# Kernel optimization log

Hardware: AMD Instinct MI355X
Metric: run time of the kernel (lower is better)

## Reference

```python
import jax, jax.numpy as jnp
import numpy as np

B, N, H, HS = 8, 96, 8, 32
NS = H * HS  # 256, also ES
EPS = 1e-5


def _linear(x, w, b):
    return x @ w + b  # w: [in, out]


def _ln(x, g, b):
    m = jnp.mean(x, axis=-1, keepdims=True)
    v = jnp.var(x, axis=-1, keepdims=True)
    return (x - m) * jax.lax.rsqrt(v + EPS) * g + b


def _sep_n(x):  # [B,N,NS] -> [B,H,N,HS]
    b, n, _ = x.shape
    return x.reshape(b, n, H, HS).transpose(0, 2, 1, 3)


def _sep_e(x):  # [B,N,N,ES] -> [B,H,N,N,HS]
    b, n, _, _ = x.shape
    return x.reshape(b, n, n, H, HS).transpose(0, 3, 1, 2, 4)


def setup_inputs() -> dict:
    key = jax.random.key(0)
    ks = jax.random.split(key, 32)
    s = 1.0 / np.sqrt(NS)
    d = {
        "node_tensors": jax.random.normal(ks[0], (B, N, NS), jnp.float32),
        "edge_tensors": jax.random.normal(ks[1], (B, N, N, NS), jnp.float32),
    }
    names = ["Wn", "We", "Wn1", "Wn2", "Wee"]
    for i, nm in enumerate(names):
        d[nm + "_w"] = jax.random.uniform(ks[2 + 2 * i], (3, NS, NS), jnp.float32, -s, s)
        d[nm + "_b"] = jax.random.uniform(ks[3 + 2 * i], (3, NS), jnp.float32, -s, s)
    for i, nm in enumerate(["NL1", "NL2", "EL1", "EL2"]):
        d[nm + "_w"] = jax.random.uniform(ks[12 + 2 * i], (NS, NS), jnp.float32, -s, s)
        d[nm + "_b"] = jax.random.uniform(ks[13 + 2 * i], (NS,), jnp.float32, -s, s)
    d["NLN1_g"] = jnp.ones((NS,), jnp.float32)
    d["NLN1_b"] = jnp.zeros((NS,), jnp.float32)
    d["ELN1_g"] = jnp.ones((NS,), jnp.float32)
    d["ELN1_b"] = jnp.zeros((NS,), jnp.float32)
    return d


def _forward(node_tensors, edge_tensors, Wn_w, Wn_b, We_w, We_b, Wn1_w, Wn1_b,
             Wn2_w, Wn2_b, Wee_w, Wee_b, NL1_w, NL1_b, NL2_w, NL2_b,
             EL1_w, EL1_b, EL2_w, EL2_b, NLN1_g, NLN1_b, ELN1_g, ELN1_b):
    scale = 1.0 / jnp.sqrt(jnp.float32(HS))
    b = node_tensors.shape[0]

    # --- node attention ---
    eQ = _sep_e(_linear(edge_tensors, We_w[0], We_b[0]))
    eK = _sep_e(_linear(edge_tensors, We_w[1], We_b[1]))
    eV = _sep_e(_linear(edge_tensors, We_w[2], We_b[2]))
    nQ = _sep_n(_linear(node_tensors, Wn_w[0], Wn_b[0]))
    nK = _sep_n(_linear(node_tensors, Wn_w[1], Wn_b[1]))
    nV = _sep_n(_linear(node_tensors, Wn_w[2], Wn_b[2]))

    Q = eQ + nQ[:, :, :, None, :]          # [B,H,N,N,HS]
    K = eK + nK[:, :, None, :, :]
    scores = jnp.einsum('bhijc,bhijc->bhij', Q, K) * scale
    attn = jax.nn.softmax(scores, axis=-1)
    V = eV + nV[:, :, None, :, :]
    new_nodes = jnp.einsum('bhij,bhijc->bhic', attn, V)   # [B,H,N,HS]
    attw = new_nodes.transpose(0, 2, 1, 3).reshape(b, N, NS)

    res = _linear(jax.nn.relu(_linear(attw, NL1_w, NL1_b)), NL2_w, NL2_b)
    node_out = _ln(node_tensors + res, NLN1_g, NLN1_b)

    # --- edge update ---
    n1Q = _sep_n(_linear(node_out, Wn1_w[0], Wn1_b[0]))
    n1K = _sep_n(_linear(node_out, Wn1_w[1], Wn1_b[1]))
    n1V = _sep_n(_linear(node_out, Wn1_w[2], Wn1_b[2]))
    n2Q = _sep_n(_linear(node_out, Wn2_w[0], Wn2_b[0]))
    n2K = _sep_n(_linear(node_out, Wn2_w[1], Wn2_b[1]))
    n2V = _sep_n(_linear(node_out, Wn2_w[2], Wn2_b[2]))
    eQe = _sep_e(_linear(edge_tensors, Wee_w[0], Wee_b[0]))
    eKe = _sep_e(_linear(edge_tensors, Wee_w[1], Wee_b[1]))
    eVe = _sep_e(_linear(edge_tensors, Wee_w[2], Wee_b[2]))

    Qe = eQe + n1Q[:, :, :, None, :] + n2Q[:, :, None, :, :]
    Ke = eKe + n1K[:, :, :, None, :] + n2K[:, :, None, :, :]
    se = jnp.einsum('bhijc,bhijc->bhij', Qe, Ke) * scale
    attn_e = jax.nn.silu(se)                               # [B,H,N,N]
    Ve = eVe + n1V[:, :, :, None, :] + n2V[:, :, None, :, :]
    new_edges = attn_e[..., None] * Ve                     # [B,H,N,N,HS]
    attw_e = new_edges.transpose(0, 2, 3, 1, 4).reshape(b, N, N, NS)

    res_e = _linear(jax.nn.relu(_linear(attw_e, EL1_w, EL1_b)), EL2_w, EL2_b)
    edge_out = _ln(edge_tensors + res_e, ELN1_g, ELN1_b)
    return node_out, edge_out


def reference(node_tensors, edge_tensors, Wn_w, Wn_b, We_w, We_b, Wn1_w, Wn1_b,
              Wn2_w, Wn2_b, Wee_w, Wee_b, NL1_w, NL1_b, NL2_w, NL2_b,
              EL1_w, EL1_b, EL2_w, EL2_b, NLN1_g, NLN1_b, ELN1_g, ELN1_b):
    return _forward(node_tensors, edge_tensors, Wn_w, Wn_b, We_w, We_b,
                    Wn1_w, Wn1_b, Wn2_w, Wn2_b, Wee_w, Wee_b, NL1_w, NL1_b,
                    NL2_w, NL2_b, EL1_w, EL1_b, EL2_w, EL2_b,
                    NLN1_g, NLN1_b, ELN1_g, ELN1_b)
```

## Files before the change

### kernel.cpp

```cpp
#include <hip/hip_runtime.h>


#define DI __device__ __forceinline__

typedef float f32x4 __attribute__((ext_vector_type(4)));
typedef short bf16x8 __attribute__((ext_vector_type(8)));

DI unsigned short f2bf(float f) {
  union { float f; unsigned u; } v; v.f = f;
  return (unsigned short)((v.u + 0x7FFFu + ((v.u >> 16) & 1u)) >> 16);
}
DI float bf2f(unsigned short h) {
  union { unsigned u; float f; } v; v.u = ((unsigned)h) << 16;
  return v.f;
}

#define LDE 264
#define SCALE 0.17677669529663687f

#define MFMA(A, B, C) __builtin_amdgcn_mfma_f32_16x16x32_bf16((A), (B), (C), 0, 0, 0)

__global__ __launch_bounds__(256)
void prep_frags(const float* __restrict__ We_w, const float* __restrict__ Wee_w,
                const float* __restrict__ EL1_w, const float* __restrict__ EL2_w,
                const float* __restrict__ NL1_w, const float* __restrict__ NL2_w,
                const float* __restrict__ Wn1_w, const float* __restrict__ Wn2_w,
                const float* __restrict__ Wn_w,
                unsigned short* __restrict__ fb)
{
  __shared__ float Wl[32 * 256];
  const int t = threadIdx.x;
  const int blk = blockIdx.x, kt = blk & 7, ms = blk >> 3;
  const float* src; unsigned short* dst; int NT, ntbase;
  if (ms < 3)       { src = We_w  + ms * 65536;        dst = fb;           NT = 48; ntbase = ms * 16; }
  else if (ms < 6)  { src = Wee_w + (ms - 3) * 65536;  dst = fb + 196608;  NT = 48; ntbase = (ms - 3) * 16; }
  else if (ms == 6) { src = EL1_w;                     dst = fb + 393216;  NT = 16; ntbase = 0; }
  else if (ms == 7) { src = EL2_w;                     dst = fb + 458752;  NT = 16; ntbase = 0; }
  else if (ms == 8) { src = NL1_w;                     dst = fb + 524288;  NT = 16; ntbase = 0; }
  else if (ms == 9) { src = NL2_w;                     dst = fb + 589824;  NT = 16; ntbase = 0; }
  else if (ms < 13) { src = Wn1_w + (ms - 10) * 65536; dst = fb + 655360;  NT = 48; ntbase = (ms - 10) * 16; }
  else if (ms < 16) { src = Wn2_w + (ms - 13) * 65536; dst = fb + 851968;  NT = 48; ntbase = (ms - 13) * 16; }
  else              { src = Wn_w  + (ms - 16) * 65536; dst = fb + 1048576; NT = 48; ntbase = (ms - 16) * 16; }
  for (int u = t; u < 32 * 64; u += 256) {
    const int r = u >> 6, c4 = (u & 63) << 2;
    *(float4*)(Wl + r * 256 + c4) = *(const float4*)(src + (kt * 32 + r) * 256 + c4);
  }
  __syncthreads();
  for (int u = t; u < 16 * 64; u += 256) {
    const int ntl = u >> 6, l = u & 63;
    const int kb = (l >> 4) << 3, c = ntl * 16 + (l & 15);
    unsigned short tmp[8];
    #pragma unroll
    for (int i = 0; i < 8; ++i) tmp[i] = f2bf(Wl[(kb + i) * 256 + c]);
    const int nt = ntbase + ntl;
    *(uint4*)(dst + ((size_t)(kt * NT + nt) * 64 + l) * 8) = *(const uint4*)tmp;
  }
}

__global__ __launch_bounds__(256)
void node_qkv(const float* __restrict__ node, const unsigned short* __restrict__ WnF,
              const float* __restrict__ Wb, float* __restrict__ nQ,
              float* __restrict__ nK, float* __restrict__ nV)
{
  __shared__ unsigned short Xl[16 * LDE];
  const int t = threadIdx.x, lane = t & 63, w = t >> 6;
  const int rb = blockIdx.x, r0 = rb * 16;
  const int b = rb / 6, nbase = (rb % 6) * 16;

  for (int u = t; u < 16 * 64; u += 256) {
    const int j = u >> 6, gg = u & 63;
    const float4 v = *(const float4*)(node + (size_t)(r0 + j) * 256 + gg * 4);
    const unsigned lo = (unsigned)f2bf(v.x) | ((unsigned)f2bf(v.y) << 16);
    const unsigned hi = (unsigned)f2bf(v.z) | ((unsigned)f2bf(v.w) << 16);
    *(uint2*)(Xl + j * LDE + gg * 4) = make_uint2(lo, hi);
  }
  __syncthreads();

  const f32x4 z = {0.f, 0.f, 0.f, 0.f};
  bf16x8 xfr[8];
  #pragma unroll
  for (int kt = 0; kt < 8; ++kt)
    xfr[kt] = *(const bf16x8*)(Xl + (lane & 15) * LDE + ((lane >> 4) << 3) + kt * 32);
  f32x4 ac[12] = {z, z, z, z, z, z, z, z, z, z, z, z};
  __builtin_amdgcn_s_setprio(1);
  for (int kt = 0; kt < 8; ++kt) {
    #pragma unroll
    for (int m = 0; m < 12; ++m) {
      const int nt = w * 12 + m;
      const bf16x8 bf = *(const bf16x8*)(WnF + ((kt * 48 + nt) * 64 + lane) * 8);
      ac[m] = MFMA(xfr[kt], bf, ac[m]);
    }
  }
  __builtin_amdgcn_s_setprio(0);
  #pragma unroll
  for (int m = 0; m < 12; ++m) {
    const int colg = (w * 12 + m) * 16 + (lane & 15);
    const int q = colg >> 8, cn = colg & 255, h = cn >> 5, c = cn & 31;
    float* o = (q == 0) ? nQ : (q == 1) ? nK : nV;
    const float bv = Wb[colg];
    #pragma unroll
    for (int r = 0; r < 4; ++r) {
      const int j = ((lane >> 4) << 2) + r;
      o[((b * 8 + h) * 96 + nbase + j) * 32 + c] = ac[m][r] + bv;
    }
  }
}

__global__ __launch_bounds__(512, 2)
void node_attn(const float* __restrict__ edge, const float* __restrict__ We_b,
               const unsigned short* __restrict__ WeF,
               const float* __restrict__ nQ, const float* __restrict__ nK,
               const float* __restrict__ nV, float* __restrict__ attw)
{
  __shared__ unsigned short Elds[96 * LDE];
  __shared__ float sc[768];
  __shared__ float nQp[256];
  __shared__ float bias[768];

  const int tid = threadIdx.x, lane = tid & 63, wid = tid >> 6;
  const int b = blockIdx.x & 7, i = blockIdx.x >> 3;
  const size_t bi = (size_t)(b * 96 + i);

  if (tid < 256) nQp[tid] = nQ[((b * 8 + (tid >> 5)) * 96 + i) * 32 + (tid & 31)];
  for (int u = tid; u < 768; u += 512) bias[u] = We_b[u];

  const float* Erow = edge + bi * 24576;
  for (int u = tid; u < 96 * 64; u += 512) {
    const int j = u >> 6, g = u & 63;
    const float4 v = *(const float4*)(Erow + j * 256 + g * 4);
    const unsigned lo = (unsigned)f2bf(v.x) | ((unsigned)f2bf(v.y) << 16);
    const unsigned hi = (unsigned)f2bf(v.z) | ((unsigned)f2bf(v.w) << 16);
    *(uint2*)(Elds + j * LDE + g * 4) = make_uint2(lo, hi);
  }
  __syncthreads();

  {
    const int h = wid;
    const unsigned short* wq0 = WeF + ((2 * h) * 64 + lane) * 8;
    const unsigned short* wq1 = WeF + ((2 * h + 1) * 64 + lane) * 8;
    const unsigned short* wk0 = WeF + ((16 + 2 * h) * 64 + lane) * 8;
    const unsigned short* wk1 = WeF + ((17 + 2 * h) * 64 + lane) * 8;
    const int c0 = h * 32 + (lane & 15), c1 = c0 + 16;
    const float qb0 = bias[c0] + nQp[c0], qb1 = bias[c1] + nQp[c1];
    const float kb0 = bias[256 + c0], kb1 = bias[256 + c1];
    for (int pass = 0; pass < 2; ++pass) {
      const f32x4 z = {0.f, 0.f, 0.f, 0.f};
      f32x4 aq0[3] = {z, z, z}, aq1[3] = {z, z, z}, ak0[3] = {z, z, z}, ak1[3] = {z, z, z};
      __builtin_amdgcn_s_setprio(1);
      for (int kt = 0; kt < 8; ++kt) {
        const bf16x8 b0 = *(const bf16x8*)(wq0 + kt * 24576);
        const bf16x8 b1 = *(const bf16x8*)(wq1 + kt * 24576);
        const bf16x8 b2 = *(const bf16x8*)(wk0 + kt * 24576);
        const bf16x8 b3 = *(const bf16x8*)(wk1 + kt * 24576);
        #pragma unroll
        for (int m = 0; m < 3; ++m) {
          const int mt = pass * 3 + m;
          const bf16x8 afr = *(const bf16x8*)(Elds + (mt * 16 + (lane & 15)) * LDE
                                              + ((lane >> 4) << 3) + kt * 32);
          aq0[m] = MFMA(afr, b0, aq0[m]);
          aq1[m] = MFMA(afr, b1, aq1[m]);
          ak0[m] = MFMA(afr, b2, ak0[m]);
          ak1[m] = MFMA(afr, b3, ak1[m]);
        }
      }
      __builtin_amdgcn_s_setprio(0);
      #pragma unroll
      for (int m = 0; m < 3; ++m) {
        const int mt = pass * 3 + m;
        float prod[4];
        #pragma unroll
        for (int r = 0; r < 4; ++r) {
          const int j = mt * 16 + ((lane >> 4) << 2) + r;
          const int g = ((b * 8 + h) * 96 + j) * 32;
          const float k0v = ak0[m][r] + kb0 + nK[g + (lane & 15)];
          const float k1v = ak1[m][r] + kb1 + nK[g + 16 + (lane & 15)];
          prod[r] = (aq0[m][r] + qb0) * k0v + (aq1[m][r] + qb1) * k1v;
        }
        #pragma unroll
        for (int mm = 1; mm < 16; mm <<= 1) {
          #pragma unroll
          for (int r = 0; r < 4; ++r) prod[r] += __shfl_xor(prod[r], mm, 64);
        }
        if ((lane & 15) == 0) {
          #pragma unroll
          for (int r = 0; r < 4; ++r)
            sc[h * 96 + mt * 16 + ((lane >> 4) << 2) + r] = prod[r];
        }
      }
    }
  }

  const f32x4 z = {0.f, 0.f, 0.f, 0.f};
  f32x4 accB[6][2] = {{z, z}, {z, z}, {z, z}, {z, z}, {z, z}, {z, z}};
  const int col0 = wid * 16 + (lane & 15), col1 = col0 + 128;
  const int h0 = col0 >> 5, cc0 = col0 & 31;
  const int h1 = col1 >> 5, cc1 = col1 & 31;
  {
    const unsigned short* wb0 = WeF + ((32 + wid) * 64 + lane) * 8;
    const unsigned short* wb1 = WeF + ((40 + wid) * 64 + lane) * 8;
    __builtin_amdgcn_s_setprio(1);
    for (int kt = 0; kt < 8; ++kt) {
      const bf16x8 b0 = *(const bf16x8*)(wb0 + kt * 24576);
      const bf16x8 b1 = *(const bf16x8*)(wb1 + kt * 24576);
      #pragma unroll
      for (int mt = 0; mt < 6; ++mt) {
        const bf16x8 afr = *(const bf16x8*)(Elds + (mt * 16 + (lane & 15)) * LDE
                                            + ((lane >> 4) << 3) + kt * 32);
        accB[mt][0] = MFMA(afr, b0, accB[mt][0]);
        accB[mt][1] = MFMA(afr, b1, accB[mt][1]);
      }
    }
    __builtin_amdgcn_s_setprio(0);
    const float base0 = bias[512 + col0], base1 = bias[512 + col1];
    #pragma unroll
    for (int mt = 0; mt < 6; ++mt) {
      #pragma unroll
      for (int r = 0; r < 4; ++r) {
        const int j = mt * 16 + ((lane >> 4) << 2) + r;
        accB[mt][0][r] += base0 + nV[((b * 8 + h0) * 96 + j) * 32 + cc0];
        accB[mt][1][r] += base1 + nV[((b * 8 + h1) * 96 + j) * 32 + cc1];
      }
    }
  }

  {
    const int h = wid;
    const float s0 = sc[h * 96 + lane] * SCALE;
    const float s1 = (lane < 32) ? sc[h * 96 + 64 + lane] * SCALE : -1e30f;
    float mx = fmaxf(s0, s1);
    #pragma unroll
    for (int m = 1; m < 64; m <<= 1) mx = fmaxf(mx, __shfl_xor(mx, m, 64));
    const float e0 = __expf(s0 - mx);
    const float e1 = (lane < 32) ? __expf(s1 - mx) : 0.f;
    float sm = e0 + e1;
    #pragma unroll
    for (int m = 1; m < 64; m <<= 1) sm += __shfl_xor(sm, m, 64);
    const float inv = 1.f / sm;
    sc[h * 96 + lane] = e0 * inv;
    if (lane < 32) sc[h * 96 + 64 + lane] = e1 * inv;
  }
  __syncthreads();

  {
    float nn[2] = {0.f, 0.f};
    #pragma unroll
    for (int mt = 0; mt < 6; ++mt) {
      #pragma unroll
      for (int r = 0; r < 4; ++r) {
        const int j = mt * 16 + ((lane >> 4) << 2) + r;
        nn[0] += sc[h0 * 96 + j] * accB[mt][0][r];
        nn[1] += sc[h1 * 96 + j] * accB[mt][1][r];
      }
    }
    #pragma unroll
    for (int s = 0; s < 2; ++s) {
      nn[s] += __shfl_xor(nn[s], 16, 64);
      nn[s] += __shfl_xor(nn[s], 32, 64);
    }
    if (lane < 16) {
      attw[bi * 256 + wid * 16 + lane] = nn[0];
      attw[bi * 256 + (wid + 8) * 16 + lane] = nn[1];
    }
  }
}

__global__ __launch_bounds__(256)
void node_tail(const float* __restrict__ attw, const float* __restrict__ node,
               const unsigned short* __restrict__ NL1F, const float* __restrict__ B1,
               const unsigned short* __restrict__ NL2F, const float* __restrict__ B2,
               const float* __restrict__ g, const float* __restrict__ be,
               const unsigned short* __restrict__ Wn1F, const float* __restrict__ P1b,
               const unsigned short* __restrict__ Wn2F, const float* __restrict__ P2b,
               float* __restrict__ node_out,
               float* __restrict__ n1Q, float* __restrict__ n1K, float* __restrict__ n1V,
               float* __restrict__ n2Q, float* __restrict__ n2K, float* __restrict__ n2V)
{
  __shared__ unsigned short Xl[16 * LDE];
  __shared__ unsigned short Hl[16 * LDE];
  __shared__ float bb[1024];
  __shared__ float psum[4][16], psq[4][16];
  __shared__ float statm[16], statr[16];

  const int t = threadIdx.x, lane = t & 63, w = t >> 6;
  const int ps = blockIdx.x & 1, rb = blockIdx.x >> 1;
  const int r0 = rb * 16, b = rb / 6, nbase = (rb % 6) * 16;

  bb[t] = B1[t]; bb[256 + t] = B2[t]; bb[512 + t] = g[t]; bb[768 + t] = be[t];

  for (int u = t; u < 16 * 64; u += 256) {
    const int j = u >> 6, gg = u & 63;
    const float4 v = *(const float4*)(attw + (size_t)(r0 + j) * 256 + gg * 4);
    const unsigned lo = (unsigned)f2bf(v.x) | ((unsigned)f2bf(v.y) << 16);
    const unsigned hi = (unsigned)f2bf(v.z) | ((unsigned)f2bf(v.w) << 16);
    *(uint2*)(Xl + j * LDE + gg * 4) = make_uint2(lo, hi);
  }
  __syncthreads();

  const f32x4 z = {0.f, 0.f, 0.f, 0.f};

  {
    f32x4 a1[4] = {z, z, z, z};
    for (int kt = 0; kt < 8; ++kt) {
      const bf16x8 afr = *(const bf16x8*)(Xl + (lane & 15) * LDE + ((lane >> 4) << 3) + kt * 32);
      #pragma unroll
      for (int p = 0; p < 4; ++p) {
        const bf16x8 bf = *(const bf16x8*)(NL1F + (((kt << 4) + (w * 4 + p)) * 64 + lane) * 8);
        a1[p] = MFMA(afr, bf, a1[p]);
      }
    }
    #pragma unroll
    for (int p = 0; p < 4; ++p) {
      const int col = (w * 4 + p) * 16 + (lane & 15);
      const float bv = bb[col];
      #pragma unroll
      for (int r = 0; r < 4; ++r) {
        const int j = ((lane >> 4) << 2) + r;
        Hl[j * LDE + col] = f2bf(fmaxf(a1[p][r] + bv, 0.f));
      }
    }
  }
  __syncthreads();

  float xv[4][4];
  {
    f32x4 a2[4] = {z, z, z, z};
    for (int kt = 0; kt < 8; ++kt) {
      const bf16x8 afr = *(const bf16x8*)(Hl + (lane & 15) * LDE + ((lane >> 4) << 3) + kt * 32);
      #pragma unroll
      for (int p = 0; p < 4; ++p) {
        const bf16x8 bf = *(const bf16x8*)(NL2F + (((kt << 4) + (w * 4 + p)) * 64 + lane) * 8);
        a2[p] = MFMA(afr, bf, a2[p]);
      }
    }
    #pragma unroll
    for (int p = 0; p < 4; ++p) {
      const int col = (w * 4 + p) * 16 + (lane & 15);
      const float bv = bb[256 + col];
      #pragma unroll
      for (int r = 0; r < 4; ++r) {
        const int j = ((lane >> 4) << 2) + r;
        xv[p][r] = a2[p][r] + bv + node[(size_t)(r0 + j) * 256 + col];
      }
    }
    #pragma unroll
    for (int r = 0; r < 4; ++r) {
      float s = 0.f, q = 0.f;
      #pragma unroll
      for (int p = 0; p < 4; ++p) { s += xv[p][r]; q += xv[p][r] * xv[p][r]; }
      #pragma unroll
      for (int m = 1; m < 16; m <<= 1) { s += __shfl_xor(s, m, 64); q += __shfl_xor(q, m, 64); }
      if ((lane & 15) == 0) {
        const int rl = ((lane >> 4) << 2) + r;
        psum[w][rl] = s; psq[w][rl] = q;
      }
    }
  }
  __syncthreads();
  if (t < 16) {
    const float s = psum[0][t] + psum[1][t] + psum[2][t] + psum[3][t];
    const float q = psq[0][t] + psq[1][t] + psq[2][t] + psq[3][t];
    const float mean = s * (1.f / 256.f);
    statm[t] = mean;
    statr[t] = rsqrtf(q * (1.f / 256.f) - mean * mean + 1e-5f);
  }
  __syncthreads();
  #pragma unroll
  for (int p = 0; p < 4; ++p) {
    const int col = (w * 4 + p) * 16 + (lane & 15);
    const float gv = bb[512 + col], bv = bb[768 + col];
    #pragma unroll
    for (int r = 0; r < 4; ++r) {
      const int j = ((lane >> 4) << 2) + r;
      const float o = (xv[p][r] - statm[j]) * statr[j] * gv + bv;
      if (ps == 0) node_out[(size_t)(r0 + j) * 256 + col] = o;
      Xl[j * LDE + col] = f2bf(o);
    }
  }
  __syncthreads();

  {
    const unsigned short* WF = ps ? Wn2F : Wn1F;
    const float* pb = ps ? P2b : P1b;
    bf16x8 xfr[8];
    #pragma unroll
    for (int kt = 0; kt < 8; ++kt)
      xfr[kt] = *(const bf16x8*)(Xl + (lane & 15) * LDE + ((lane >> 4) << 3) + kt * 32);
    f32x4 ac[12] = {z, z, z, z, z, z, z, z, z, z, z, z};
    __builtin_amdgcn_s_setprio(1);
    for (int kt = 0; kt < 8; ++kt) {
      #pragma unroll
      for (int m = 0; m < 12; ++m) {
        const int nt = w * 12 + m;
        const bf16x8 bf = *(const bf16x8*)(WF + ((kt * 48 + nt) * 64 + lane) * 8);
        ac[m] = MFMA(xfr[kt], bf, ac[m]);
      }
    }
    __builtin_amdgcn_s_setprio(0);
    #pragma unroll
    for (int m = 0; m < 12; ++m) {
      const int colg = (w * 12 + m) * 16 + (lane & 15);
      const int q = colg >> 8, cn = colg & 255, h = cn >> 5, c = cn & 31;
      float* o = (q == 0) ? (ps ? n2Q : n1Q)
               : (q == 1) ? (ps ? n2K : n1K)
                          : (ps ? n2V : n1V);
      const float bv = pb[colg];
      #pragma unroll
      for (int r = 0; r < 4; ++r) {
        const int j = ((lane >> 4) << 2) + r;
        o[((b * 8 + h) * 96 + nbase + j) * 32 + c] = ac[m][r] + bv;
      }
    }
  }
}

__global__ __launch_bounds__(512, 2)
void edge_update(const float* __restrict__ edge, const float* __restrict__ Wee_b,
                 const unsigned short* __restrict__ WeeF,
                 const unsigned short* __restrict__ EL1F,
                 const unsigned short* __restrict__ EL2F,
                 const float* __restrict__ EL1_b, const float* __restrict__ EL2_b,
                 const float* __restrict__ n1Q, const float* __restrict__ n1K, const float* __restrict__ n1V,
                 const float* __restrict__ n2Q, const float* __restrict__ n2K, const float* __restrict__ n2V,
                 const float* __restrict__ lng, const float* __restrict__ lnb,
                 float* __restrict__ edge_out)
{
  __shared__ unsigned short Elds[96 * LDE];
  __shared__ float se[768];
  __shared__ float bn1[768];
  __shared__ float b12[512];
  __shared__ float lg[256], lb[256];

  const int tid = threadIdx.x, lane = tid & 63, wid = tid >> 6;
  const int b = blockIdx.x & 7, i = blockIdx.x >> 3;
  const size_t bi = (size_t)(b * 96 + i);

  for (int u = tid; u < 768; u += 512) {
    const int q = u >> 8, cn = u & 255, h = cn >> 5, c = cn & 31;
    const float* s = (q == 0) ? n1Q : (q == 1) ? n1K : n1V;
    bn1[u] = Wee_b[u] + s[((b * 8 + h) * 96 + i) * 32 + c];
  }
  b12[tid] = (tid < 256) ? EL1_b[tid] : EL2_b[tid - 256];
  if (tid < 256) { lg[tid] = lng[tid]; lb[tid] = lnb[tid]; }

  const float* Erow = edge + bi * 24576;
  for (int u = tid; u < 96 * 64; u += 512) {
    const int j = u >> 6, g = u & 63;
    const float4 v = *(const float4*)(Erow + j * 256 + g * 4);
    const unsigned lo = (unsigned)f2bf(v.x) | ((unsigned)f2bf(v.y) << 16);
    const unsigned hi = (unsigned)f2bf(v.z) | ((unsigned)f2bf(v.w) << 16);
    *(uint2*)(Elds + j * LDE + g * 4) = make_uint2(lo, hi);
  }
  __syncthreads();

  {
    const int h = wid;
    const unsigned short* wq0 = WeeF + ((2 * h) * 64 + lane) * 8;
    const unsigned short* wq1 = WeeF + ((2 * h + 1) * 64 + lane) * 8;
    const unsigned short* wk0 = WeeF + ((16 + 2 * h) * 64 + lane) * 8;
    const unsigned short* wk1 = WeeF + ((17 + 2 * h) * 64 + lane) * 8;
    const int c0 = h * 32 + (lane & 15), c1 = c0 + 16;
    const float qb0 = bn1[c0], qb1 = bn1[c1];
    const float kb0 = bn1[256 + c0], kb1 = bn1[256 + c1];
    for (int pass = 0; pass < 2; ++pass) {
      const f32x4 z = {0.f, 0.f, 0.f, 0.f};
      f32x4 aq0[3] = {z, z, z}, aq1[3] = {z, z, z}, ak0[3] = {z, z, z}, ak1[3] = {z, z, z};
      __builtin_amdgcn_s_setprio(1);
      for (int kt = 0; kt < 8; ++kt) {
        const bf16x8 b0 = *(const bf16x8*)(wq0 + kt * 24576);
        const bf16x8 b1 = *(const bf16x8*)(wq1 + kt * 24576);
        const bf16x8 b2 = *(const bf16x8*)(wk0 + kt * 24576);
        const bf16x8 b3 = *(const bf16x8*)(wk1 + kt * 24576);
        #pragma unroll
        for (int m = 0; m < 3; ++m) {
          const int mt = pass * 3 + m;
          const bf16x8 afr = *(const bf16x8*)(Elds + (mt * 16 + (lane & 15)) * LDE
                                              + ((lane >> 4) << 3) + kt * 32);
          aq0[m] = MFMA(afr, b0, aq0[m]);
          aq1[m] = MFMA(afr, b1, aq1[m]);
          ak0[m] = MFMA(afr, b2, ak0[m]);
          ak1[m] = MFMA(afr, b3, ak1[m]);
        }
      }
      __builtin_amdgcn_s_setprio(0);
      #pragma unroll
      for (int m = 0; m < 3; ++m) {
        const int mt = pass * 3 + m;
        float prod[4];
        #pragma unroll
        for (int r = 0; r < 4; ++r) {
          const int j = mt * 16 + ((lane >> 4) << 2) + r;
          const int g = ((b * 8 + h) * 96 + j) * 32;
          const float q0v = aq0[m][r] + qb0 + n2Q[g + (lane & 15)];
          const float q1v = aq1[m][r] + qb1 + n2Q[g + 16 + (lane & 15)];
          const float k0v = ak0[m][r] + kb0 + n2K[g + (lane & 15)];
          const float k1v = ak1[m][r] + kb1 + n2K[g + 16 + (lane & 15)];
          prod[r] = q0v * k0v + q1v * k1v;
        }
        #pragma unroll
        for (int mm = 1; mm < 16; mm <<= 1) {
          #pragma unroll
          for (int r = 0; r < 4; ++r) prod[r] += __shfl_xor(prod[r], mm, 64);
        }
        if ((lane & 15) == 0) {
          #pragma unroll
          for (int r = 0; r < 4; ++r) {
            const float d = prod[r] * SCALE;
            se[h * 96 + mt * 16 + ((lane >> 4) << 2) + r] = d / (1.f + __expf(-d));
          }
        }
      }
    }
  }

  const f32x4 z = {0.f, 0.f, 0.f, 0.f};
  f32x4 acc[6][2] = {{z, z}, {z, z}, {z, z}, {z, z}, {z, z}, {z, z}};
  const int col0 = wid * 16 + (lane & 15), col1 = col0 + 128;
  {
    const int h0 = col0 >> 5, cc0 = col0 & 31;
    const int h1 = col1 >> 5, cc1 = col1 & 31;
    const unsigned short* wb0 = WeeF + ((32 + wid) * 64 + lane) * 8;
    const unsigned short* wb1 = WeeF + ((40 + wid) * 64 + lane) * 8;
    __builtin_amdgcn_s_setprio(1);
    for (int kt = 0; kt < 8; ++kt) {
      const bf16x8 b0 = *(const bf16x8*)(wb0 + kt * 24576);
      const bf16x8 b1 = *(const bf16x8*)(wb1 + kt * 24576);
      #pragma unroll
      for (int mt = 0; mt < 6; ++mt) {
        const bf16x8 afr = *(const bf16x8*)(Elds + (mt * 16 + (lane & 15)) * LDE
                                            + ((lane >> 4) << 3) + kt * 32);
        acc[mt][0] = MFMA(afr, b0, acc[mt][0]);
        acc[mt][1] = MFMA(afr, b1, acc[mt][1]);
      }
    }
    __builtin_amdgcn_s_setprio(0);
    const float base0 = bn1[512 + col0], base1 = bn1[512 + col1];
    #pragma unroll
    for (int mt = 0; mt < 6; ++mt) {
      #pragma unroll
      for (int r = 0; r < 4; ++r) {
        const int j = mt * 16 + ((lane >> 4) << 2) + r;
        acc[mt][0][r] += base0 + n2V[((b * 8 + h0) * 96 + j) * 32 + cc0];
        acc[mt][1][r] += base1 + n2V[((b * 8 + h1) * 96 + j) * 32 + cc1];
      }
    }
  }
  __syncthreads();

  {
    const int h0 = col0 >> 5, h1 = col1 >> 5;
    #pragma unroll
    for (int mt = 0; mt < 6; ++mt) {
      #pragma unroll
      for (int r = 0; r < 4; ++r) {
        const int j = mt * 16 + ((lane >> 4) << 2) + r;
        Elds[j * LDE + col0] = f2bf(se[h0 * 96 + j] * acc[mt][0][r]);
        Elds[j * LDE + col1] = f2bf(se[h1 * 96 + j] * acc[mt][1][r]);
      }
    }
  }
  __syncthreads();

  {
    #pragma unroll
    for (int mt = 0; mt < 6; ++mt) { acc[mt][0] = z; acc[mt][1] = z; }
    const unsigned short* wb0 = EL1F + (wid * 64 + lane) * 8;
    const unsigned short* wb1 = EL1F + ((wid + 8) * 64 + lane) * 8;
    __builtin_amdgcn_s_setprio(1);
    for (int kt = 0; kt < 8; ++kt) {
      const bf16x8 b0 = *(const bf16x8*)(wb0 + kt * 8192);
      const bf16x8 b1 = *(const bf16x8*)(wb1 + kt * 8192);
      #pragma unroll
      for (int mt = 0; mt < 6; ++mt) {
        const bf16x8 afr = *(const bf16x8*)(Elds + (mt * 16 + (lane & 15)) * LDE
                                            + ((lane >> 4) << 3) + kt * 32);
        acc[mt][0] = MFMA(afr, b0, acc[mt][0]);
        acc[mt][1] = MFMA(afr, b1, acc[mt][1]);
      }
    }
    __builtin_amdgcn_s_setprio(0);
    __syncthreads();
    const float bv0 = b12[col0], bv1 = b12[col1];
    #pragma unroll
    for (int mt = 0; mt < 6; ++mt) {
      #pragma unroll
      for (int r = 0; r < 4; ++r) {
        const int j = mt * 16 + ((lane >> 4) << 2) + r;
        Elds[j * LDE + col0] = f2bf(fmaxf(acc[mt][0][r] + bv0, 0.f));
        Elds[j * LDE + col1] = f2bf(fmaxf(acc[mt][1][r] + bv1, 0.f));
      }
    }
  }
  __syncthreads();

  {
    #pragma unroll
    for (int mt = 0; mt < 6; ++mt) { acc[mt][0] = z; acc[mt][1] = z; }
    const unsigned short* wb0 = EL2F + (wid * 64 + lane) * 8;
    const unsigned short* wb1 = EL2F + ((wid + 8) * 64 + lane) * 8;
    __builtin_amdgcn_s_setprio(1);
    for (int kt = 0; kt < 8; ++kt) {
      const bf16x8 b0 = *(const bf16x8*)(wb0 + kt * 8192);
      const bf16x8 b1 = *(const bf16x8*)(wb1 + kt * 8192);
      #pragma unroll
      for (int mt = 0; mt < 6; ++mt) {
        const bf16x8 afr = *(const bf16x8*)(Elds + (mt * 16 + (lane & 15)) * LDE
                                            + ((lane >> 4) << 3) + kt * 32);
        acc[mt][0] = MFMA(afr, b0, acc[mt][0]);
        acc[mt][1] = MFMA(afr, b1, acc[mt][1]);
      }
    }
    __builtin_amdgcn_s_setprio(0);
    const float bv0 = b12[256 + col0], bv1 = b12[256 + col1];
    const float g0 = lg[col0], g1 = lg[col1], be0 = lb[col0], be1 = lb[col1];
    #pragma unroll
    for (int mt = 0; mt < 6; ++mt) {
      #pragma unroll
      for (int r = 0; r < 4; ++r) {
        const int j = mt * 16 + ((lane >> 4) << 2) + r;
        acc[mt][0][r] += bv0 + Erow[j * 256 + col0];
        acc[mt][1][r] += bv1 + Erow[j * 256 + col1];
      }
    }
    #pragma unroll
    for (int mt = 0; mt < 6; ++mt) {
      #pragma unroll
      for (int r = 0; r < 4; ++r) {
        float s = acc[mt][0][r] + acc[mt][1][r];
        float q = acc[mt][0][r] * acc[mt][0][r] + acc[mt][1][r] * acc[mt][1][r];
        #pragma unroll
        for (int m = 1; m < 16; m <<= 1) { s += __shfl_xor(s, m, 64); q += __shfl_xor(q, m, 64); }
        if ((lane & 15) == 0) {
          const int j = mt * 16 + ((lane >> 4) << 2) + r;
          se[wid * 96 + j] = s; bn1[wid * 96 + j] = q;
        }
      }
    }
    __syncthreads();
    if (tid < 96) {
      float s = 0.f, q = 0.f;
      #pragma unroll
      for (int w = 0; w < 8; ++w) { s += se[w * 96 + tid]; q += bn1[w * 96 + tid]; }
      const float mean = s * (1.f / 256.f);
      b12[tid] = mean;
      b12[96 + tid] = rsqrtf(q * (1.f / 256.f) - mean * mean + 1e-5f);
    }
    __syncthreads();
    float* orow = edge_out + bi * 24576;
    #pragma unroll
    for (int mt = 0; mt < 6; ++mt) {
      #pragma unroll
      for (int r = 0; r < 4; ++r) {
        const int j = mt * 16 + ((lane >> 4) << 2) + r;
        const float mean = b12[j], rs = b12[96 + j];
        orow[j * 256 + col0] = (acc[mt][0][r] - mean) * rs * g0 + be0;
        orow[j * 256 + col1] = (acc[mt][1][r] - mean) * rs * g1 + be1;
      }
    }
  }
}

extern "C" void kernel_launch(void* const* d_in, const int* in_sizes, int n_in,
                              void* d_out, int out_size, void* d_ws, size_t ws_size,
                              hipStream_t stream)
{
  (void)in_sizes; (void)n_in; (void)out_size; (void)ws_size;

  const float* node   = (const float*)d_in[0];
  const float* edge   = (const float*)d_in[1];
  const float* Wn_w   = (const float*)d_in[2];
  const float* Wn_b   = (const float*)d_in[3];
  const float* We_w   = (const float*)d_in[4];
  const float* We_b   = (const float*)d_in[5];
  const float* Wn1_w  = (const float*)d_in[6];
  const float* Wn1_b  = (const float*)d_in[7];
  const float* Wn2_w  = (const float*)d_in[8];
  const float* Wn2_b  = (const float*)d_in[9];
  const float* Wee_w  = (const float*)d_in[10];
  const float* Wee_b  = (const float*)d_in[11];
  const float* NL1_w  = (const float*)d_in[12];
  const float* NL1_b  = (const float*)d_in[13];
  const float* NL2_w  = (const float*)d_in[14];
  const float* NL2_b  = (const float*)d_in[15];
  const float* EL1_w  = (const float*)d_in[16];
  const float* EL1_b  = (const float*)d_in[17];
  const float* EL2_w  = (const float*)d_in[18];
  const float* EL2_b  = (const float*)d_in[19];
  const float* NLN1_g = (const float*)d_in[20];
  const float* NLN1_b = (const float*)d_in[21];
  const float* ELN1_g = (const float*)d_in[22];
  const float* ELN1_b = (const float*)d_in[23];

  float* out = (float*)d_out;
  float* node_out = out;
  float* edge_out = out + 196608;

  float* wsf = (float*)d_ws;
  float* nQ  = wsf;                float* nK  = wsf + 196608;   float* nV  = wsf + 393216;
  float* n1Q = wsf + 589824;       float* n1K = wsf + 786432;   float* n1V = wsf + 983040;
  float* n2Q = wsf + 1179648;      float* n2K = wsf + 1376256;  float* n2V = wsf + 1572864;
  float* attw = wsf + 1769472;
  unsigned short* fb   = (unsigned short*)(wsf + 1966080);
  unsigned short* WeF  = fb;
  unsigned short* WeeF = fb + 196608;
  unsigned short* EL1F = fb + 393216;
  unsigned short* EL2F = fb + 458752;
  unsigned short* NL1F = fb + 524288;
  unsigned short* NL2F = fb + 589824;
  unsigned short* Wn1F = fb + 655360;
  unsigned short* Wn2F = fb + 851968;
  unsigned short* WnF  = fb + 1048576;

  prep_frags<<<152, 256, 0, stream>>>(We_w, Wee_w, EL1_w, EL2_w, NL1_w, NL2_w,
                                      Wn1_w, Wn2_w, Wn_w, fb);
  node_qkv<<<48, 256, 0, stream>>>(node, WnF, Wn_b, nQ, nK, nV);
  node_attn<<<768, 512, 0, stream>>>(edge, We_b, WeF, nQ, nK, nV, attw);
  node_tail<<<96, 256, 0, stream>>>(attw, node, NL1F, NL1_b, NL2F, NL2_b,
                                    NLN1_g, NLN1_b, Wn1F, Wn1_b, Wn2F, Wn2_b,
                                    node_out, n1Q, n1K, n1V, n2Q, n2K, n2V);
  edge_update<<<768, 512, 0, stream>>>(edge, Wee_b, WeeF, EL1F, EL2F,
                                       EL1_b, EL2_b, n1Q, n1K, n1V,
                                       n2Q, n2K, n2V, ELN1_g, ELN1_b, edge_out);
}
```

Baseline: 250.8 us.

## Split edge_update into half-row blocks of 256 threads with wider per-wave tiles

The edge_update kernel now launches 1536 blocks of 256 threads. Each block handles 48 of the 96 j-rows for one (b,i) pair instead of all 96 with 512 threads. Each wave processes two heads in the attention-score step and four 16-column tiles in the GEMMs, which reuses each A fragment across more MFMAs and halves LDS per block so more blocks fit per CU. The trade-offs are higher register pressure from 12 accumulators per wave and weight fragments being reloaded by twice as many blocks.

```diff
diff --git a/kernel.cpp b/kernel.cpp
--- a/kernel.cpp
+++ b/kernel.cpp
@@ -413,7 +413,7 @@
   }
 }
 
-__global__ __launch_bounds__(512, 2)
+__global__ __launch_bounds__(256, 4)
 void edge_update(const float* __restrict__ edge, const float* __restrict__ Wee_b,
                  const unsigned short* __restrict__ WeeF,
                  const unsigned short* __restrict__ EL1F,
@@ -424,26 +424,27 @@
                  const float* __restrict__ lng, const float* __restrict__ lnb,
                  float* __restrict__ edge_out)
 {
-  __shared__ unsigned short Elds[96 * LDE];
-  __shared__ float se[768];
+  __shared__ unsigned short Elds[48 * LDE];
+  __shared__ float se[384];
   __shared__ float bn1[768];
   __shared__ float b12[512];
   __shared__ float lg[256], lb[256];
 
-  const int tid = threadIdx.x, lane = tid & 63, wid = tid >> 6;
-  const int b = blockIdx.x & 7, i = blockIdx.x >> 3;
+  const int tid = threadIdx.x, lane = tid & 63, w = tid >> 6;
+  const int b = blockIdx.x & 7, rest = blockIdx.x >> 3;
+  const int i = rest >> 1, jt = rest & 1, jbase = jt * 48;
   const size_t bi = (size_t)(b * 96 + i);
 
-  for (int u = tid; u < 768; u += 512) {
+  for (int u = tid; u < 768; u += 256) {
     const int q = u >> 8, cn = u & 255, h = cn >> 5, c = cn & 31;
     const float* s = (q == 0) ? n1Q : (q == 1) ? n1K : n1V;
     bn1[u] = Wee_b[u] + s[((b * 8 + h) * 96 + i) * 32 + c];
   }
-  b12[tid] = (tid < 256) ? EL1_b[tid] : EL2_b[tid - 256];
-  if (tid < 256) { lg[tid] = lng[tid]; lb[tid] = lnb[tid]; }
-
-  const float* Erow = edge + bi * 24576;
-  for (int u = tid; u < 96 * 64; u += 512) {
+  b12[tid] = EL1_b[tid]; b12[256 + tid] = EL2_b[tid];
+  lg[tid] = lng[tid]; lb[tid] = lnb[tid];
+
+  const float* Erow = edge + bi * 24576 + jbase * 256;
+  for (int u = tid; u < 48 * 64; u += 256) {
     const int j = u >> 6, g = u & 63;
     const float4 v = *(const float4*)(Erow + j * 256 + g * 4);
     const unsigned lo = (unsigned)f2bf(v.x) | ((unsigned)f2bf(v.y) << 16);
@@ -452,8 +453,8 @@
   }
   __syncthreads();
 
-  {
-    const int h = wid;
+  for (int pp = 0; pp < 2; ++pp) {
+    const int h = w + (pp << 2);
     const unsigned short* wq0 = WeeF + ((2 * h) * 64 + lane) * 8;
     const unsigned short* wq1 = WeeF + ((2 * h + 1) * 64 + lane) * 8;
     const unsigned short* wk0 = WeeF + ((16 + 2 * h) * 64 + lane) * 8;
@@ -461,199 +462,210 @@
     const int c0 = h * 32 + (lane & 15), c1 = c0 + 16;
     const float qb0 = bn1[c0], qb1 = bn1[c1];
     const float kb0 = bn1[256 + c0], kb1 = bn1[256 + c1];
-    for (int pass = 0; pass < 2; ++pass) {
-      const f32x4 z = {0.f, 0.f, 0.f, 0.f};
-      f32x4 aq0[3] = {z, z, z}, aq1[3] = {z, z, z}, ak0[3] = {z, z, z}, ak1[3] = {z, z, z};
-      __builtin_amdgcn_s_setprio(1);
-      for (int kt = 0; kt < 8; ++kt) {
-        const bf16x8 b0 = *(const bf16x8*)(wq0 + kt * 24576);
-        const bf16x8 b1 = *(const bf16x8*)(wq1 + kt * 24576);
-        const bf16x8 b2 = *(const bf16x8*)(wk0 + kt * 24576);
-        const bf16x8 b3 = *(const bf16x8*)(wk1 + kt * 24576);
-        #pragma unroll
-        for (int m = 0; m < 3; ++m) {
-          const int mt = pass * 3 + m;
-          const bf16x8 afr = *(const bf16x8*)(Elds + (mt * 16 + (lane & 15)) * LDE
-                                              + ((lane >> 4) << 3) + kt * 32);
-          aq0[m] = MFMA(afr, b0, aq0[m]);
-          aq1[m] = MFMA(afr, b1, aq1[m]);
-          ak0[m] = MFMA(afr, b2, ak0[m]);
-          ak1[m] = MFMA(afr, b3, ak1[m]);
-        }
-      }
-      __builtin_amdgcn_s_setprio(0);
-      #pragma unroll
-      for (int m = 0; m < 3; ++m) {
-        const int mt = pass * 3 + m;
-        float prod[4];
-        #pragma unroll
-        for (int r = 0; r < 4; ++r) {
-          const int j = mt * 16 + ((lane >> 4) << 2) + r;
-          const int g = ((b * 8 + h) * 96 + j) * 32;
-          const float q0v = aq0[m][r] + qb0 + n2Q[g + (lane & 15)];
-          const float q1v = aq1[m][r] + qb1 + n2Q[g + 16 + (lane & 15)];
-          const float k0v = ak0[m][r] + kb0 + n2K[g + (lane & 15)];
-          const float k1v = ak1[m][r] + kb1 + n2K[g + 16 + (lane & 15)];
-          prod[r] = q0v * k0v + q1v * k1v;
-        }
-        #pragma unroll
-        for (int mm = 1; mm < 16; mm <<= 1) {
-          #pragma unroll
-          for (int r = 0; r < 4; ++r) prod[r] += __shfl_xor(prod[r], mm, 64);
-        }
-        if ((lane & 15) == 0) {
-          #pragma unroll
-          for (int r = 0; r < 4; ++r) {
-            const float d = prod[r] * SCALE;
-            se[h * 96 + mt * 16 + ((lane >> 4) << 2) + r] = d / (1.f + __expf(-d));
-          }
-        }
-      }
-    }
-  }
-
-  const f32x4 z = {0.f, 0.f, 0.f, 0.f};
-  f32x4 acc[6][2] = {{z, z}, {z, z}, {z, z}, {z, z}, {z, z}, {z, z}};
-  const int col0 = wid * 16 + (lane & 15), col1 = col0 + 128;
-  {
-    const int h0 = col0 >> 5, cc0 = col0 & 31;
-    const int h1 = col1 >> 5, cc1 = col1 & 31;
-    const unsigned short* wb0 = WeeF + ((32 + wid) * 64 + lane) * 8;
-    const unsigned short* wb1 = WeeF + ((40 + wid) * 64 + lane) * 8;
+    const f32x4 z = {0.f, 0.f, 0.f, 0.f};
+    f32x4 aq0[3] = {z, z, z}, aq1[3] = {z, z, z}, ak0[3] = {z, z, z}, ak1[3] = {z, z, z};
     __builtin_amdgcn_s_setprio(1);
     for (int kt = 0; kt < 8; ++kt) {
-      const bf16x8 b0 = *(const bf16x8*)(wb0 + kt * 24576);
-      const bf16x8 b1 = *(const bf16x8*)(wb1 + kt * 24576);
-      #pragma unroll
-      for (int mt = 0; mt < 6; ++mt) {
-        const bf16x8 afr = *(const bf16x8*)(Elds + (mt * 16 + (lane & 15)) * LDE
+      const bf16x8 b0 = *(const bf16x8*)(wq0 + kt * 24576);
+      const bf16x8 b1 = *(const bf16x8*)(wq1 + kt * 24576);
+      const bf16x8 b2 = *(const bf16x8*)(wk0 + kt * 24576);
+      const bf16x8 b3 = *(const bf16x8*)(wk1 + kt * 24576);
+      #pragma unroll
+      for (int m = 0; m < 3; ++m) {
+        const bf16x8 afr = *(const bf16x8*)(Elds + (m * 16 + (lane & 15)) * LDE
                                             + ((lane >> 4) << 3) + kt * 32);
-        acc[mt][0] = MFMA(afr, b0, acc[mt][0]);
-        acc[mt][1] = MFMA(afr, b1, acc[mt][1]);
+        aq0[m] = MFMA(afr, b0, aq0[m]);
+        aq1[m] = MFMA(afr, b1, aq1[m]);
+        ak0[m] = MFMA(afr, b2, ak0[m]);
+        ak1[m] = MFMA(afr, b3, ak1[m]);
       }
     }
     __builtin_amdgcn_s_setprio(0);
-    const float base0 = bn1[512 + col0], base1 = bn1[512 + col1];
-    #pragma unroll
-    for (int mt = 0; mt < 6; ++mt) {
+    #pragma unroll
+    for (int m = 0; m < 3; ++m) {
+      float prod[4];
       #pragma unroll
       for (int r = 0; r < 4; ++r) {
-        const int j = mt * 16 + ((lane >> 4) << 2) + r;
-        acc[mt][0][r] += base0 + n2V[((b * 8 + h0) * 96 + j) * 32 + cc0];
-        acc[mt][1][r] += base1 + n2V[((b * 8 + h1) * 96 + j) * 32 + cc1];
-      }
-    }
-  }
-  __syncthreads();
-
-  {
-    const int h0 = col0 >> 5, h1 = col1 >> 5;
-    #pragma unroll
-    for (int mt = 0; mt < 6; ++mt) {
-      #pragma unroll
-      for (int r = 0; r < 4; ++r) {
-        const int j = mt * 16 + ((lane >> 4) << 2) + r;
-        Elds[j * LDE + col0] = f2bf(se[h0 * 96 + j] * acc[mt][0][r]);
-        Elds[j * LDE + col1] = f2bf(se[h1 * 96 + j] * acc[mt][1][r]);
-      }
-    }
-  }
-  __syncthreads();
-
-  {
-    #pragma unroll
-    for (int mt = 0; mt < 6; ++mt) { acc[mt][0] = z; acc[mt][1] = z; }
-    const unsigned short* wb0 = EL1F + (wid * 64 + lane) * 8;
-    const unsigned short* wb1 = EL1F + ((wid + 8) * 64 + lane) * 8;
+        const int jl = m * 16 + ((lane >> 4) << 2) + r;
+        const int g = ((b * 8 + h) * 96 + jbase + jl) * 32;
+        const float q0v = aq0[m][r] + qb0 + n2Q[g + (lane & 15)];
+        const float q1v = aq1[m][r] + qb1 + n2Q[g + 16 + (lane & 15)];
+        const float k0v = ak0[m][r] + kb0 + n2K[g + (lane & 15)];
+        const float k1v = ak1[m][r] + kb1 + n2K[g + 16 + (lane & 15)];
+        prod[r] = q0v * k0v + q1v * k1v;
+      }
+      #pragma unroll
+      for (int mm = 1; mm < 16; mm <<= 1) {
+        #pragma unroll
+        for (int r = 0; r < 4; ++r) prod[r] += __shfl_xor(prod[r], mm, 64);
+      }
+      if ((lane & 15) == 0) {
+        #pragma unroll
+        for (int r = 0; r < 4; ++r) {
+          const float d = prod[r] * SCALE;
+          se[h * 48 + m * 16 + ((lane >> 4) << 2) + r] = d / (1.f + __expf(-d));
+        }
+      }
+    }
+  }
+
+  const f32x4 z = {0.f, 0.f, 0.f, 0.f};
+  f32x4 acc[3][4] = {{z, z, z, z}, {z, z, z, z}, {z, z, z, z}};
+  int col[4], colh[4];
+  #pragma unroll
+  for (int c = 0; c < 4; ++c) { col[c] = (w + (c << 2)) * 16 + (lane & 15); colh[c] = col[c] >> 5; }
+  {
     __builtin_amdgcn_s_setprio(1);
     for (int kt = 0; kt < 8; ++kt) {
-      const bf16x8 b0 = *(const bf16x8*)(wb0 + kt * 8192);
-      const bf16x8 b1 = *(const bf16x8*)(wb1 + kt * 8192);
-      #pragma unroll
-      for (int mt = 0; mt < 6; ++mt) {
-        const bf16x8 afr = *(const bf16x8*)(Elds + (mt * 16 + (lane & 15)) * LDE
+      bf16x8 bfr[4];
+      #pragma unroll
+      for (int c = 0; c < 4; ++c)
+        bfr[c] = *(const bf16x8*)(WeeF + (((32 + w + (c << 2)) * 64 + lane) * 8) + kt * 24576);
+      #pragma unroll
+      for (int m = 0; m < 3; ++m) {
+        const bf16x8 afr = *(const bf16x8*)(Elds + (m * 16 + (lane & 15)) * LDE
                                             + ((lane >> 4) << 3) + kt * 32);
-        acc[mt][0] = MFMA(afr, b0, acc[mt][0]);
-        acc[mt][1] = MFMA(afr, b1, acc[mt][1]);
+        #pragma unroll
+        for (int c = 0; c < 4; ++c) acc[m][c] = MFMA(afr, bfr[c], acc[m][c]);
+      }
+    }
+    __builtin_amdgcn_s_setprio(0);
+    #pragma unroll
+    for (int c = 0; c < 4; ++c) {
+      const int cc = col[c] & 31;
+      const float base = bn1[512 + col[c]];
+      #pragma unroll
+      for (int m = 0; m < 3; ++m) {
+        #pragma unroll
+        for (int r = 0; r < 4; ++r) {
+          const int jl = m * 16 + ((lane >> 4) << 2) + r;
+          acc[m][c][r] += base + n2V[((b * 8 + colh[c]) * 96 + jbase + jl) * 32 + cc];
+        }
+      }
+    }
+  }
+  __syncthreads();
+
+  #pragma unroll
+  for (int c = 0; c < 4; ++c) {
+    #pragma unroll
+    for (int m = 0; m < 3; ++m) {
+      #pragma unroll
+      for (int r = 0; r < 4; ++r) {
+        const int jl = m * 16 + ((lane >> 4) << 2) + r;
+        Elds[jl * LDE + col[c]] = f2bf(se[colh[c] * 48 + jl] * acc[m][c][r]);
+      }
+    }
+  }
+  __syncthreads();
+
+  {
+    #pragma unroll
+    for (int m = 0; m < 3; ++m)
+      #pragma unroll
+      for (int c = 0; c < 4; ++c) acc[m][c] = z;
+    __builtin_amdgcn_s_setprio(1);
+    for (int kt = 0; kt < 8; ++kt) {
+      bf16x8 bfr[4];
+      #pragma unroll
+      for (int c = 0; c < 4; ++c)
+        bfr[c] = *(const bf16x8*)(EL1F + (((w + (c << 2)) * 64 + lane) * 8) + kt * 8192);
+      #pragma unroll
+      for (int m = 0; m < 3; ++m) {
+        const bf16x8 afr = *(const bf16x8*)(Elds + (m * 16 + (lane & 15)) * LDE
+                                            + ((lane >> 4) << 3) + kt * 32);
+        #pragma unroll
+        for (int c = 0; c < 4; ++c) acc[m][c] = MFMA(afr, bfr[c], acc[m][c]);
       }
     }
     __builtin_amdgcn_s_setprio(0);
     __syncthreads();
-    const float bv0 = b12[col0], bv1 = b12[col1];
-    #pragma unroll
-    for (int mt = 0; mt < 6; ++mt) {
-      #pragma unroll
-      for (int r = 0; r < 4; ++r) {
-        const int j = mt * 16 + ((lane >> 4) << 2) + r;
-        Elds[j * LDE + col0] = f2bf(fmaxf(acc[mt][0][r] + bv0, 0.f));
-        Elds[j * LDE + col1] = f2bf(fmaxf(acc[mt][1][r] + bv1, 0.f));
-      }
-    }
-  }
-  __syncthreads();
-
-  {
-    #pragma unroll
-    for (int mt = 0; mt < 6; ++mt) { acc[mt][0] = z; acc[mt][1] = z; }
-    const unsigned short* wb0 = EL2F + (wid * 64 + lane) * 8;
-    const unsigned short* wb1 = EL2F + ((wid + 8) * 64 + lane) * 8;
+    #pragma unroll
+    for (int c = 0; c < 4; ++c) {
+      const float bv = b12[col[c]];
+      #pragma unroll
+      for (int m = 0; m < 3; ++m) {
+        #pragma unroll
+        for (int r = 0; r < 4; ++r) {
+          const int jl = m * 16 + ((lane >> 4) << 2) + r;
+          Elds[jl * LDE + col[c]] = f2bf(fmaxf(acc[m][c][r] + bv, 0.f));
+        }
+      }
+    }
+  }
+  __syncthreads();
+
+  {
+    #pragma unroll
+    for (int m = 0; m < 3; ++m)
+      #pragma unroll
+      for (int c = 0; c < 4; ++c) acc[m][c] = z;
     __builtin_amdgcn_s_setprio(1);
     for (int kt = 0; kt < 8; ++kt) {
-      const bf16x8 b0 = *(const bf16x8*)(wb0 + kt * 8192);
-      const bf16x8 b1 = *(const bf16x8*)(wb1 + kt * 8192);
-      #pragma unroll
-      for (int mt = 0; mt < 6; ++mt) {
-        const bf16x8 afr = *(const bf16x8*)(Elds + (mt * 16 + (lane & 15)) * LDE
+      bf16x8 bfr[4];
+      #pragma unroll
+      for (int c = 0; c < 4; ++c)
+        bfr[c] = *(const bf16x8*)(EL2F + (((w + (c << 2)) * 64 + lane) * 8) + kt * 8192);
+      #pragma unroll
+      for (int m = 0; m < 3; ++m) {
+        const bf16x8 afr = *(const bf16x8*)(Elds + (m * 16 + (lane & 15)) * LDE
                                             + ((lane >> 4) << 3) + kt * 32);
-        acc[mt][0] = MFMA(afr, b0, acc[mt][0]);
-        acc[mt][1] = MFMA(afr, b1, acc[mt][1]);
+        #pragma unroll
+        for (int c = 0; c < 4; ++c) acc[m][c] = MFMA(afr, bfr[c], acc[m][c]);
       }
     }
     __builtin_amdgcn_s_setprio(0);
-    const float bv0 = b12[256 + col0], bv1 = b12[256 + col1];
-    const float g0 = lg[col0], g1 = lg[col1], be0 = lb[col0], be1 = lb[col1];
-    #pragma unroll
-    for (int mt = 0; mt < 6; ++mt) {
+    #pragma unroll
+    for (int c = 0; c < 4; ++c) {
+      const float bv = b12[256 + col[c]];
+      #pragma unroll
+      for (int m = 0; m < 3; ++m) {
+        #pragma unroll
+        for (int r = 0; r < 4; ++r) {
+          const int jl = m * 16 + ((lane >> 4) << 2) + r;
+          acc[m][c][r] += bv + Erow[jl * 256 + col[c]];
+        }
+      }
+    }
+    #pragma unroll
+    for (int m = 0; m < 3; ++m) {
       #pragma unroll
       for (int r = 0; r < 4; ++r) {
-        const int j = mt * 16 + ((lane >> 4) << 2) + r;
-        acc[mt][0][r] += bv0 + Erow[j * 256 + col0];
-        acc[mt][1][r] += bv1 + Erow[j * 256 + col1];
-      }
-    }
-    #pragma unroll
-    for (int mt = 0; mt < 6; ++mt) {
-      #pragma unroll
-      for (int r = 0; r < 4; ++r) {
-        float s = acc[mt][0][r] + acc[mt][1][r];
-        float q = acc[mt][0][r] * acc[mt][0][r] + acc[mt][1][r] * acc[mt][1][r];
-        #pragma unroll
-        for (int m = 1; m < 16; m <<= 1) { s += __shfl_xor(s, m, 64); q += __shfl_xor(q, m, 64); }
+        float s = 0.f, q = 0.f;
+        #pragma unroll
+        for (int c = 0; c < 4; ++c) {
+          s += acc[m][c][r];
+          q += acc[m][c][r] * acc[m][c][r];
+        }
+        #pragma unroll
+        for (int mm = 1; mm < 16; mm <<= 1) { s += __shfl_xor(s, mm, 64); q += __shfl_xor(q, mm, 64); }
         if ((lane & 15) == 0) {
-          const int j = mt * 16 + ((lane >> 4) << 2) + r;
-          se[wid * 96 + j] = s; bn1[wid * 96 + j] = q;
+          const int jl = m * 16 + ((lane >> 4) << 2) + r;
+          se[w * 48 + jl] = s; bn1[w * 48 + jl] = q;
         }
       }
     }
     __syncthreads();
-    if (tid < 96) {
+    if (tid < 48) {
       float s = 0.f, q = 0.f;
       #pragma unroll
-      for (int w = 0; w < 8; ++w) { s += se[w * 96 + tid]; q += bn1[w * 96 + tid]; }
+      for (int wv = 0; wv < 4; ++wv) { s += se[wv * 48 + tid]; q += bn1[wv * 48 + tid]; }
       const float mean = s * (1.f / 256.f);
       b12[tid] = mean;
-      b12[96 + tid] = rsqrtf(q * (1.f / 256.f) - mean * mean + 1e-5f);
+      b12[48 + tid] = rsqrtf(q * (1.f / 256.f) - mean * mean + 1e-5f);
     }
     __syncthreads();
-    float* orow = edge_out + bi * 24576;
-    #pragma unroll
-    for (int mt = 0; mt < 6; ++mt) {
-      #pragma unroll
-      for (int r = 0; r < 4; ++r) {
-        const int j = mt * 16 + ((lane >> 4) << 2) + r;
-        const float mean = b12[j], rs = b12[96 + j];
-        orow[j * 256 + col0] = (acc[mt][0][r] - mean) * rs * g0 + be0;
-        orow[j * 256 + col1] = (acc[mt][1][r] - mean) * rs * g1 + be1;
+    float* orow = edge_out + bi * 24576 + jbase * 256;
+    #pragma unroll
+    for (int c = 0; c < 4; ++c) {
+      const float gv = lg[col[c]], bvv = lb[col[c]];
+      #pragma unroll
+      for (int m = 0; m < 3; ++m) {
+        #pragma unroll
+        for (int r = 0; r < 4; ++r) {
+          const int jl = m * 16 + ((lane >> 4) << 2) + r;
+          orow[jl * 256 + col[c]] = (acc[m][c][r] - b12[jl]) * b12[48 + jl] * gv + bvv;
+        }
       }
     }
   }
@@ -717,7 +729,7 @@
   node_tail<<<96, 256, 0, stream>>>(attw, node, NL1F, NL1_b, NL2F, NL2_b,
                                     NLN1_g, NLN1_b, Wn1F, Wn1_b, Wn2F, Wn2_b,
                                     node_out, n1Q, n1K, n1V, n2Q, n2K, n2V);
-  edge_update<<<768, 512, 0, stream>>>(edge, Wee_b, WeeF, EL1F, EL2F,
-                                       EL1_b, EL2_b, n1Q, n1K, n1V,
-                                       n2Q, n2K, n2V, ELN1_g, ELN1_b, edge_out);
+  edge_update<<<1536, 256, 0, stream>>>(edge, Wee_b, WeeF, EL1F, EL2F,
+                                        EL1_b, EL2_b, n1Q, n1K, n1V,
+                                        n2Q, n2K, n2V, ELN1_g, ELN1_b, edge_out);
 }
```

New measurement: 293.1 us. 16.9% more time.
